# Kernel optimization log

Measured on AMD Instinct MI355X. Metric: run time of the kernel, lower is better.

The kernel has to match this reference:

```python
import jax, jax.numpy as jnp
import numpy as np

DIM = 1024
NUM_HEADS = 16
HEAD_DIM = DIM // NUM_HEADS
SCALE = DIM ** (-0.5)  # NOTE: original scales by full dim, not head_dim


def setup_inputs() -> dict:
    key = jax.random.key(0)
    ks = jax.random.split(key, 5)
    B, S = 2, 2048
    x = jax.random.normal(ks[0], (B, S, DIM), dtype=jnp.float32)
    w_qkv = jax.random.normal(ks[1], (DIM, 3 * DIM), dtype=jnp.float32) * (DIM ** -0.5)
    b_qkv = jax.random.normal(ks[2], (3 * DIM,), dtype=jnp.float32) * 0.02
    w_proj = jax.random.normal(ks[3], (DIM, DIM), dtype=jnp.float32) * (DIM ** -0.5)
    b_proj = jax.random.normal(ks[4], (DIM,), dtype=jnp.float32) * 0.02
    return {"x": x, "w_qkv": w_qkv, "b_qkv": b_qkv, "w_proj": w_proj, "b_proj": b_proj}


def reference(x, w_qkv, b_qkv, w_proj, b_proj):
    B, S, D = x.shape
    qkv = x @ w_qkv + b_qkv                                  # [B,S,3D]
    qkv = qkv.reshape(B, S, NUM_HEADS, 3 * HEAD_DIM).transpose(0, 2, 1, 3)  # [B,H,S,3hd]
    q, k, v = jnp.split(qkv, 3, axis=-1)                     # each [B,H,S,hd]
    attn = jnp.einsum("bhqd,bhkd->bhqk", q, k) * SCALE       # [B,H,S,S]
    attn = jax.nn.softmax(attn, axis=-1)
    out = jnp.einsum("bhqk,bhkd->bhqd", attn, v)             # [B,H,S,hd]
    out = out.transpose(0, 2, 1, 3).reshape(B, S, D)
    return out @ w_proj + b_proj
```

## Files before the change

### kernel.cpp

```cpp
#include <hip/hip_runtime.h>
#include <hip/hip_bf16.h>

#define DIM 1024
#define NH 16
#define HD 64
#define BB 2
#define SS 2048
#define MROWS (BB * SS)
#define SCALE 0.03125f
#define SC_LOG2E 0.04508422002778011f

typedef unsigned short u16;
typedef unsigned int u32;
typedef __attribute__((ext_vector_type(8))) short short8;
typedef __attribute__((ext_vector_type(4))) float f32x4;
typedef __attribute__((ext_vector_type(2))) unsigned int u32x2;

#if __has_builtin(__builtin_amdgcn_exp2f)
#define EXP2(x) __builtin_amdgcn_exp2f(x)
#else
#define EXP2(x) __builtin_exp2f(x)
#endif

__device__ __forceinline__ u16 f2bf(float f) {
  union { float f; u32 u; } v; v.f = f;
  return (u16)((v.u + 0x7fffu + ((v.u >> 16) & 1u)) >> 16);
}

__device__ __forceinline__ u32 pack2bf(float a, float b) {
  union { __hip_bfloat162 h; u32 u; } cv;
  cv.h = __float22bfloat162_rn(make_float2(a, b));
  return cv.u;
}

__device__ __forceinline__ void plswap32(u32& a, u32& b) {
#if __has_builtin(__builtin_amdgcn_permlane32_swap)
  u32x2 t = __builtin_amdgcn_permlane32_swap(a, b, false, false);
  a = t[0]; b = t[1];
#else
  asm("v_permlane32_swap_b32 %0, %1" : "+v"(a), "+v"(b));
#endif
}
__device__ __forceinline__ void plswap16(u32& a, u32& b) {
#if __has_builtin(__builtin_amdgcn_permlane16_swap)
  u32x2 t = __builtin_amdgcn_permlane16_swap(a, b, false, false);
  a = t[0]; b = t[1];
#else
  asm("v_permlane16_swap_b32 %0, %1" : "+v"(a), "+v"(b));
#endif
}

__device__ __forceinline__ void async16(const u16* g, u16* l) {
  __builtin_amdgcn_global_load_lds(
      (const __attribute__((address_space(1))) void*)(const void*)g,
      (__attribute__((address_space(3))) void*)(void*)l, 16, 0, 0);
}

__device__ __forceinline__ short8 ld8(const u16* p) { return *(const short8*)p; }

__global__ void cvt_kernel(const float* __restrict__ in, u16* __restrict__ out, int n4) {
  int i = blockIdx.x * blockDim.x + threadIdx.x;
  if (i < n4) {
    float4 v = ((const float4*)in)[i];
    u32 lo = (u32)f2bf(v.x) | ((u32)f2bf(v.y) << 16);
    u32 hi = (u32)f2bf(v.z) | ((u32)f2bf(v.w) << 16);
    ((uint2*)out)[i] = make_uint2(lo, hi);
  }
}

__global__ void tconv_kernel(const float* __restrict__ in, u16* __restrict__ out, int R, int C) {
  __shared__ u16 t[64 * 65];
  int c0 = blockIdx.x * 64, r0 = blockIdx.y * 64;
  #pragma unroll
  for (int i = 0; i < 16; i++) {
    int j = i * 256 + threadIdx.x;
    int rr = j >> 6, cc = j & 63;
    t[rr * 65 + cc] = f2bf(in[(size_t)(r0 + rr) * C + c0 + cc]);
  }
  __syncthreads();
  #pragma unroll
  for (int i = 0; i < 16; i++) {
    int j = i * 256 + threadIdx.x;
    int oc = j >> 6, orr = j & 63;
    out[(size_t)(c0 + oc) * R + r0 + orr] = t[orr * 65 + oc];
  }
}

template <int MODE, int BN, int NXB>
__global__ __launch_bounds__(256, (BN == 128 ? 2 : 3)) void gemm_bk64(
    const u16* __restrict__ A, const u16* __restrict__ Bt,
    const float* __restrict__ bias, void* __restrict__ C,
    u16* __restrict__ vT, int M, int N, int K) {
  constexpr int JN = BN / 32;
  constexpr int BTI = BN / 32;
  constexpr int BUF = 8192 + BN * 64;
  __shared__ __align__(16) u16 smem[2 * BUF];
  const int tid = threadIdx.x;
  const int w = tid >> 6, l = tid & 63;
  const int r = l & 15, q = l >> 4;
  const int nwg = gridDim.x;
  const int cpx = nwg >> 3;
  const int lin = blockIdx.x;
  const int swz = (lin & 7) * cpx + (lin >> 3);
  const int m0 = (swz / NXB) * 128, n0 = (swz % NXB) * BN;
  const int qm = (w & 1) * 64, qn = (w >> 1) * (BN / 2);

  const int gc = (l & 7) ^ (l >> 3);
  const size_t aoffb = (size_t)(m0 + w * 32 + (l >> 3)) * K + (size_t)gc * 8;
  const size_t boffb = (size_t)(n0 + w * (BN / 4) + (l >> 3)) * K + (size_t)gc * 8;
  const int xs = r & 7;

#define GSTAGE(K0, BASE) do {                                                    \
    u16* As_ = (BASE); u16* Bs_ = As_ + 8192;                                    \
    _Pragma("unroll")                                                            \
    for (int t = 0; t < 4; t++)                                                  \
      async16(A + aoffb + (size_t)t * 8 * K + (K0), As_ + w * 2048 + t * 512 + l * 8); \
    _Pragma("unroll")                                                            \
    for (int t = 0; t < BTI; t++)                                                \
      async16(Bt + boffb + (size_t)t * 8 * K + (K0), Bs_ + w * (BN * 16) + t * 512 + l * 8); \
  } while (0)

  f32x4 acc[4][JN] = {};
  GSTAGE(0, smem);
  __syncthreads();
  for (int k0 = 0; k0 < K; k0 += 64) {
    u16* As = smem + ((k0 >> 6) & 1) * BUF;
    u16* Bs = As + 8192;
    if (k0 + 64 < K) GSTAGE(k0 + 64, smem + ((((k0 >> 6) & 1) ^ 1) * BUF));
    short8 af[2][4], bfr[2][JN];
    #pragma unroll
    for (int kq = 0; kq < 2; kq++) {
      #pragma unroll
      for (int i = 0; i < 4; i++)
        af[kq][i] = ld8(&As[(qm + i * 16 + r) * 64 + (((kq * 4 + q) ^ xs) * 8)]);
      #pragma unroll
      for (int j = 0; j < JN; j++)
        bfr[kq][j] = ld8(&Bs[(qn + j * 16 + r) * 64 + (((kq * 4 + q) ^ xs) * 8)]);
    }
    #pragma unroll
    for (int kq = 0; kq < 2; kq++)
      #pragma unroll
      for (int i = 0; i < 4; i++)
        #pragma unroll
        for (int j = 0; j < JN; j++)
          acc[i][j] = __builtin_amdgcn_mfma_f32_16x16x32_bf16(af[kq][i], bfr[kq][j], acc[i][j], 0, 0, 0);
    __syncthreads();
  }
#undef GSTAGE
  #pragma unroll
  for (int i = 0; i < 4; i++) {
    int ro = m0 + qm + i * 16 + q * 4;
    #pragma unroll
    for (int j = 0; j < JN; j++) {
      int col = n0 + qn + j * 16 + r;
      float bv = bias[col];
      float v0 = acc[i][j][0] + bv, v1 = acc[i][j][1] + bv;
      float v2 = acc[i][j][2] + bv, v3 = acc[i][j][3] + bv;
      if (MODE == 1) {
        float* out = (float*)C;
        out[(size_t)(ro + 0) * N + col] = v0;
        out[(size_t)(ro + 1) * N + col] = v1;
        out[(size_t)(ro + 2) * N + col] = v2;
        out[(size_t)(ro + 3) * N + col] = v3;
      } else {
        int h = col / 192, wi = col - h * 192;
        if (wi >= 128) {
          int bb = ro >> 11, s = ro & 2047, d = wi - 128;
          uint2 pk = make_uint2(pack2bf(v0, v1), pack2bf(v2, v3));
          *(uint2*)&vT[((size_t)((bb * NH + h) * HD + d)) * SS + s] = pk;
        } else {
          u16* qk2 = (u16*)C;
          const float sc = (wi < 64) ? SC_LOG2E : 1.0f;
          qk2[(size_t)(ro + 0) * 2048 + h * 128 + wi] = f2bf(v0 * sc);
          qk2[(size_t)(ro + 1) * 2048 + h * 128 + wi] = f2bf(v1 * sc);
          qk2[(size_t)(ro + 2) * 2048 + h * 128 + wi] = f2bf(v2 * sc);
          qk2[(size_t)(ro + 3) * 2048 + h * 128 + wi] = f2bf(v3 * sc);
        }
      }
    }
  }
}

__global__ __launch_bounds__(512, 8) void attn7_kernel(
    const u16* __restrict__ qk2, const u16* __restrict__ vT,
    u16* __restrict__ attno) {
  __shared__ __align__(16) u16 smem[16384];
  const int tid = threadIdx.x;
  const int w = tid >> 6, l = tid & 63;
  const int r = l & 15, q = l >> 4;
  const int wq = w & 3, ws = w >> 2;
  const int lin = blockIdx.x + 32 * (blockIdx.y + 16 * blockIdx.z);
  const int k8 = lin & 7, jj = lin >> 3;
  const int bh = ((jj >> 5) << 3) + k8;
  const int h = bh & 15, b = bh >> 4;
  const int q0 = (jj & 31) * 64;

  const u16* qb = qk2 + (size_t)b * SS * 2048;
  const u16* kB = qb + h * 128 + 64;
  const u16* vB = vT + (size_t)((b * NH + h) * HD) * SS;

  short8 qf[2];
  #pragma unroll
  for (int kq = 0; kq < 2; kq++)
    qf[kq] = ld8(qb + (size_t)(q0 + wq * 16 + r) * 2048 + h * 128 + kq * 32 + q * 8);

  const int gch = (l & 7) ^ (l >> 3);

#define STAGE(KV0, DST) do {                                                     \
    u16* Kd_ = (DST); u16* Vd_ = Kd_ + 4096;                                     \
    async16(kB + (size_t)((KV0) + w * 8 + (l >> 3)) * 2048 + gch * 8,            \
            &Kd_[w * 512 + l * 8]);                                              \
    async16(vB + (size_t)(w * 8 + (l >> 3)) * SS + (KV0) + gch * 8,              \
            &Vd_[w * 512 + l * 8]);                                              \
  } while (0)

  const short8 vone = {0x3F80, 0x3F80, 0x3F80, 0x3F80, 0x3F80, 0x3F80, 0x3F80, 0x3F80};
  f32x4 oacc[4] = {};
  f32x4 den = {};

  STAGE(0, smem);
  __syncthreads();

  for (int t = 0; t < 32; ++t) {
    u16* Ks = smem + (t & 1) * 8192;
    u16* Vs = Ks + 4096;
    if (t < 31) STAGE((t + 1) * 64, smem + (((t & 1) ^ 1) * 8192));

    f32x4 sacc[2] = {};
    #pragma unroll
    for (int j2 = 0; j2 < 2; j2++) {
      const u16* krow = &Ks[(ws * 32 + j2 * 16 + r) * 64];
      short8 a0 = ld8(krow + ((q ^ (r & 7)) * 8));
      short8 a1 = ld8(krow + (((4 + q) ^ (r & 7)) * 8));
      __builtin_amdgcn_s_setprio(1);
      sacc[j2] = __builtin_amdgcn_mfma_f32_16x16x32_bf16(a0, qf[0], sacc[j2], 0, 0, 0);
      sacc[j2] = __builtin_amdgcn_mfma_f32_16x16x32_bf16(a1, qf[1], sacc[j2], 0, 0, 0);
      __builtin_amdgcn_s_setprio(0);
    }
    short8 pa;
    {
      u32 A0 = pack2bf(EXP2(sacc[0][0]), EXP2(sacc[0][1]));
      u32 A1 = pack2bf(EXP2(sacc[0][2]), EXP2(sacc[0][3]));
      u32 B0 = pack2bf(EXP2(sacc[1][0]), EXP2(sacc[1][1]));
      u32 B1 = pack2bf(EXP2(sacc[1][2]), EXP2(sacc[1][3]));
      plswap32(A0, B0);
      plswap32(A1, B1);
      plswap16(A0, B0);
      plswap16(A1, B1);
      union { short8 s8; u32 u[4]; } pk;
      pk.u[0] = A0; pk.u[1] = A1; pk.u[2] = B0; pk.u[3] = B1;
      pa = pk.s8;
    }
    __builtin_amdgcn_s_setprio(1);
    den = __builtin_amdgcn_mfma_f32_16x16x32_bf16(pa, vone, den, 0, 0, 0);
    #pragma unroll
    for (int dj = 0; dj < 4; dj++) {
      short8 vb = ld8(&Vs[(dj * 16 + r) * 64 + (((ws * 4 + q) ^ (r & 7)) * 8)]);
      oacc[dj] = __builtin_amdgcn_mfma_f32_16x16x32_bf16(pa, vb, oacc[dj], 0, 0, 0);
    }
    __builtin_amdgcn_s_setprio(0);
    __syncthreads();
  }
#undef STAGE

  float* part = (float*)smem;
  float* dnf  = part + 8 * 32 * 20;
  const int ho = 1 - ws;
  {
    const int wbase = (wq * 2 + ho) * 32;
    if (ws == 0) {
      *(f32x4*)&part[(wbase + r) * 20 + q * 4]      = oacc[2];
      *(f32x4*)&part[(wbase + 16 + r) * 20 + q * 4] = oacc[3];
    } else {
      *(f32x4*)&part[(wbase + r) * 20 + q * 4]      = oacc[0];
      *(f32x4*)&part[(wbase + 16 + r) * 20 + q * 4] = oacc[1];
    }
    if (r == 0)
      *(f32x4*)&dnf[(ws * 4 + wq) * 16 + q * 4] = den;
  }
  __syncthreads();
  {
    const int rbase = (wq * 2 + ws) * 32;
    f32x4 dt = *(f32x4*)&dnf[(ho * 4 + wq) * 16 + q * 4] + den;
    f32x4 oa = (ws == 0) ? oacc[0] : oacc[2];
    f32x4 ob = (ws == 0) ? oacc[1] : oacc[3];
    oa += *(f32x4*)&part[(rbase + r) * 20 + q * 4];
    ob += *(f32x4*)&part[(rbase + 16 + r) * 20 + q * 4];
    #pragma unroll
    for (int e = 0; e < 4; e++) {
      float di = 1.f / dt[e];
      int row = q0 + wq * 16 + q * 4 + e;
      u16* o = &attno[(size_t)(b * SS + row) * DIM + h * HD + ws * 32 + r];
      o[0]  = f2bf(oa[e] * di);
      o[16] = f2bf(ob[e] * di);
    }
  }
}

extern "C" void kernel_launch(void* const* d_in, const int* in_sizes, int n_in,
                              void* d_out, int out_size, void* d_ws, size_t ws_size,
                              hipStream_t stream) {
  const float* x      = (const float*)d_in[0];
  const float* w_qkv  = (const float*)d_in[1];
  const float* b_qkv  = (const float*)d_in[2];
  const float* w_proj = (const float*)d_in[3];
  const float* b_proj = (const float*)d_in[4];
  float* out = (float*)d_out;
  char* ws = (char*)d_ws;
  u16* xb     = (u16*)(ws);
  u16* wqkvT  = (u16*)(ws + ((size_t)8  << 20));
  u16* wprojT = (u16*)(ws + ((size_t)14 << 20));
  u16* qk2    = (u16*)(ws + ((size_t)16 << 20));
  u16* attno  = (u16*)(ws + ((size_t)32 << 20));
  u16* vT     = (u16*)(ws + ((size_t)40 << 20));

  cvt_kernel<<<4096, 256, 0, stream>>>(x, xb, MROWS * DIM / 4);
  tconv_kernel<<<dim3(48, 16), 256, 0, stream>>>(w_qkv, wqkvT, DIM, 3 * DIM);
  tconv_kernel<<<dim3(16, 16), 256, 0, stream>>>(w_proj, wprojT, DIM, DIM);
  gemm_bk64<0, 128, 24><<<768, 256, 0, stream>>>(xb, wqkvT, b_qkv, qk2, vT, MROWS, 3 * DIM, DIM);
  attn7_kernel<<<dim3(32, NH, BB), 512, 0, stream>>>(qk2, vT, attno);
  gemm_bk64<1, 64, 16><<<512, 256, 0, stream>>>(attno, wprojT, b_proj, out, nullptr, MROWS, DIM, DIM);
}
```

Measured before the change: 186.2 us.

## Stage only K in LDS, read V directly from global, process 128-key tiles

The attention kernel now stages only K tiles into shared memory, using the whole buffer to hold 128 keys per step instead of 64 keys of K plus V. V fragments are loaded straight from global memory inside the PV step. The loop runs 16 iterations, interleaving QK^T, exp conversion and PV over two 64-key halves, so it hits half as many barriers and can overlap more work. The trade-off is uncoalesced, latency-exposed global loads of V in the inner loop in place of LDS reads, plus more live registers from the extra accumulators and fragments.

Measured after the change: 326.6 us. +75.4%, slower.

```diff
diff --git a/kernel.cpp b/kernel.cpp
--- a/kernel.cpp
+++ b/kernel.cpp
@@ -181,7 +181,7 @@
   }
 }
 
-__global__ __launch_bounds__(512, 8) void attn7_kernel(
+__global__ __launch_bounds__(512, 8) void attn8_kernel(
     const u16* __restrict__ qk2, const u16* __restrict__ vT,
     u16* __restrict__ attno) {
   __shared__ __align__(16) u16 smem[16384];
@@ -204,14 +204,52 @@
   for (int kq = 0; kq < 2; kq++)
     qf[kq] = ld8(qb + (size_t)(q0 + wq * 16 + r) * 2048 + h * 128 + kq * 32 + q * 8);
 
-  const int gch = (l & 7) ^ (l >> 3);
+  const int klrow = l >> 3;
+  const int kchunk = (l & 7) ^ klrow;
 
 #define STAGE(KV0, DST) do {                                                     \
-    u16* Kd_ = (DST); u16* Vd_ = Kd_ + 4096;                                     \
-    async16(kB + (size_t)((KV0) + w * 8 + (l >> 3)) * 2048 + gch * 8,            \
-            &Kd_[w * 512 + l * 8]);                                              \
-    async16(vB + (size_t)(w * 8 + (l >> 3)) * SS + (KV0) + gch * 8,              \
-            &Vd_[w * 512 + l * 8]);                                              \
+    u16* Kd_ = (DST);                                                            \
+    _Pragma("unroll")                                                            \
+    for (int tt = 0; tt < 2; tt++) {                                             \
+      int g = w * 2 + tt;                                                        \
+      async16(kB + (size_t)((KV0) + g * 8 + klrow) * 2048 + kchunk * 8,          \
+              &Kd_[g * 512 + l * 8]);                                            \
+    }                                                                            \
+  } while (0)
+
+#define QKT(j2) do {                                                             \
+    const u16* krow = &Ks[(ws * 64 + (j2) * 16 + r) * 64];                       \
+    short8 a0 = ld8(krow + ((q ^ (r & 7)) * 8));                                 \
+    short8 a1 = ld8(krow + (((4 + q) ^ (r & 7)) * 8));                           \
+    __builtin_amdgcn_s_setprio(1);                                               \
+    sacc[j2] = __builtin_amdgcn_mfma_f32_16x16x32_bf16(a0, qf[0], sacc[j2], 0, 0, 0); \
+    sacc[j2] = __builtin_amdgcn_mfma_f32_16x16x32_bf16(a1, qf[1], sacc[j2], 0, 0, 0); \
+    __builtin_amdgcn_s_setprio(0);                                               \
+  } while (0)
+
+#define CONV(ks) do {                                                            \
+    u32 A0 = pack2bf(EXP2(sacc[(ks) * 2][0]), EXP2(sacc[(ks) * 2][1]));          \
+    u32 A1 = pack2bf(EXP2(sacc[(ks) * 2][2]), EXP2(sacc[(ks) * 2][3]));          \
+    u32 B0 = pack2bf(EXP2(sacc[(ks) * 2 + 1][0]), EXP2(sacc[(ks) * 2 + 1][1]));  \
+    u32 B1 = pack2bf(EXP2(sacc[(ks) * 2 + 1][2]), EXP2(sacc[(ks) * 2 + 1][3]));  \
+    plswap32(A0, B0);                                                            \
+    plswap32(A1, B1);                                                            \
+    plswap16(A0, B0);                                                            \
+    plswap16(A1, B1);                                                            \
+    union { short8 s8; u32 u[4]; } pk_;                                          \
+    pk_.u[0] = A0; pk_.u[1] = A1; pk_.u[2] = B0; pk_.u[3] = B1;                  \
+    pa[ks] = pk_.s8;                                                             \
+  } while (0)
+
+#define PV(ks) do {                                                              \
+    __builtin_amdgcn_s_setprio(1);                                               \
+    den = __builtin_amdgcn_mfma_f32_16x16x32_bf16(pa[ks], vone, den, 0, 0, 0);   \
+    _Pragma("unroll")                                                            \
+    for (int dj = 0; dj < 4; dj++) {                                             \
+      short8 vb = ld8(vB + (size_t)(dj * 16 + r) * SS + kv0 + ws * 64 + (ks) * 32 + q * 8); \
+      oacc[dj] = __builtin_amdgcn_mfma_f32_16x16x32_bf16(pa[ks], vb, oacc[dj], 0, 0, 0); \
+    }                                                                            \
+    __builtin_amdgcn_s_setprio(0);                                               \
   } while (0)
 
   const short8 vone = {0x3F80, 0x3F80, 0x3F80, 0x3F80, 0x3F80, 0x3F80, 0x3F80, 0x3F80};
@@ -221,47 +259,25 @@
   STAGE(0, smem);
   __syncthreads();
 
-  for (int t = 0; t < 32; ++t) {
+  for (int t = 0; t < 16; ++t) {
     u16* Ks = smem + (t & 1) * 8192;
-    u16* Vs = Ks + 4096;
-    if (t < 31) STAGE((t + 1) * 64, smem + (((t & 1) ^ 1) * 8192));
-
-    f32x4 sacc[2] = {};
-    #pragma unroll
-    for (int j2 = 0; j2 < 2; j2++) {
-      const u16* krow = &Ks[(ws * 32 + j2 * 16 + r) * 64];
-      short8 a0 = ld8(krow + ((q ^ (r & 7)) * 8));
-      short8 a1 = ld8(krow + (((4 + q) ^ (r & 7)) * 8));
-      __builtin_amdgcn_s_setprio(1);
-      sacc[j2] = __builtin_amdgcn_mfma_f32_16x16x32_bf16(a0, qf[0], sacc[j2], 0, 0, 0);
-      sacc[j2] = __builtin_amdgcn_mfma_f32_16x16x32_bf16(a1, qf[1], sacc[j2], 0, 0, 0);
-      __builtin_amdgcn_s_setprio(0);
-    }
-    short8 pa;
-    {
-      u32 A0 = pack2bf(EXP2(sacc[0][0]), EXP2(sacc[0][1]));
-      u32 A1 = pack2bf(EXP2(sacc[0][2]), EXP2(sacc[0][3]));
-      u32 B0 = pack2bf(EXP2(sacc[1][0]), EXP2(sacc[1][1]));
-      u32 B1 = pack2bf(EXP2(sacc[1][2]), EXP2(sacc[1][3]));
-      plswap32(A0, B0);
-      plswap32(A1, B1);
-      plswap16(A0, B0);
-      plswap16(A1, B1);
-      union { short8 s8; u32 u[4]; } pk;
-      pk.u[0] = A0; pk.u[1] = A1; pk.u[2] = B0; pk.u[3] = B1;
-      pa = pk.s8;
-    }
-    __builtin_amdgcn_s_setprio(1);
-    den = __builtin_amdgcn_mfma_f32_16x16x32_bf16(pa, vone, den, 0, 0, 0);
-    #pragma unroll
-    for (int dj = 0; dj < 4; dj++) {
-      short8 vb = ld8(&Vs[(dj * 16 + r) * 64 + (((ws * 4 + q) ^ (r & 7)) * 8)]);
-      oacc[dj] = __builtin_amdgcn_mfma_f32_16x16x32_bf16(pa, vb, oacc[dj], 0, 0, 0);
-    }
-    __builtin_amdgcn_s_setprio(0);
+    const int kv0 = t * 128;
+    if (t < 15) STAGE((t + 1) * 128, smem + (((t & 1) ^ 1) * 8192));
+
+    f32x4 sacc[4] = {};
+    short8 pa[2];
+    QKT(0); QKT(1);
+    CONV(0);
+    QKT(2); QKT(3);
+    PV(0);
+    CONV(1);
+    PV(1);
     __syncthreads();
   }
 #undef STAGE
+#undef QKT
+#undef CONV
+#undef PV
 
   float* part = (float*)smem;
   float* dnf  = part + 8 * 32 * 20;
@@ -318,6 +334,6 @@
   tconv_kernel<<<dim3(48, 16), 256, 0, stream>>>(w_qkv, wqkvT, DIM, 3 * DIM);
   tconv_kernel<<<dim3(16, 16), 256, 0, stream>>>(w_proj, wprojT, DIM, DIM);
   gemm_bk64<0, 128, 24><<<768, 256, 0, stream>>>(xb, wqkvT, b_qkv, qk2, vT, MROWS, 3 * DIM, DIM);
-  attn7_kernel<<<dim3(32, NH, BB), 512, 0, stream>>>(qk2, vT, attno);
+  attn8_kernel<<<dim3(32, NH, BB), 512, 0, stream>>>(qk2, vT, attno);
   gemm_bk64<1, 64, 16><<<512, 256, 0, stream>>>(attno, wprojT, b_proj, out, nullptr, MROWS, DIM, DIM);
 }
```
